# Kernel optimization log

Hardware: AMD Instinct MI355X
Metric: run time of the kernel (lower is better)

The kernel has to match this reference:

```python
import jax, jax.numpy as jnp
import numpy as np

L_OBS = 512                      # number_of_obs
FOV = 6.283185307179586          # full 360-degree scan
EPS_PAR = 1e-4                   # parallel-ray threshold (matches torch |rxs|<0.0001)
MAP_SIZE = 256.0
B = 8
N = 8192


def setup_inputs() -> dict:
    key = jax.random.key(0)
    k1, k2, k3 = jax.random.split(key, 3)
    # map line segments: (x3, y3, x4, y4) in [0, 256]^2
    line_seg = jax.random.uniform(k1, (N, 4), dtype=jnp.float32) * MAP_SIZE
    # poses: xy in the map interior, theta in [0, 2pi)
    xy = MAP_SIZE * 0.25 + jax.random.uniform(k2, (B, 2), dtype=jnp.float32) * (MAP_SIZE * 0.5)
    theta = jax.random.uniform(k3, (B, 1), dtype=jnp.float32) * (2.0 * np.pi)
    pose = jnp.concatenate([xy, theta], axis=-1)
    return {"line_seg": line_seg, "pose": pose}


def _sense(line_seg, pose):
    # rays(): beam angles for each pose -> [B, L]
    beam = jnp.arange(L_OBS, dtype=jnp.float32) * (FOV / L_OBS)        # [L]
    ang = beam[None, :] + pose[:, 2:3]                                  # [B, L]
    rx = jnp.cos(ang)[:, :, None]                                       # [B, L, 1]
    ry = jnp.sin(ang)[:, :, None]
    x1 = pose[:, 0][:, None, None]                                      # [B, 1, 1]
    y1 = pose[:, 1][:, None, None]

    x3 = line_seg[:, 0][None, None, :]                                  # [1, 1, N]
    y3 = line_seg[:, 1][None, None, :]
    x4 = line_seg[:, 2][None, None, :]
    y4 = line_seg[:, 3][None, None, :]
    sx = x4 - x3
    sy = y4 - y3
    x1_x3 = x1 - x3                                                     # [B, 1, N]
    y1_y3 = y1 - y3

    # ray/segment intersection parameters, broadcast to [B, L, N]
    num_a = sx * y1_y3 - sy * x1_x3
    num_b = rx * y1_y3 - ry * x1_x3
    rxs = sy * rx - sx * ry
    parallel = jnp.abs(rxs) < EPS_PAR
    safe_rxs = jnp.where(parallel, jnp.float32(1.0), rxs)
    u_a = jnp.where(parallel, jnp.float32(0.0), num_a / safe_rxs)       # [B, L, N]
    u_b = jnp.where(parallel, jnp.float32(0.0), num_b / safe_rxs)

    valid = (~parallel) & (u_b >= 0.0) & (u_b <= 1.0) & (u_a >= 0.0)
    # nearest valid hit along each ray (torch: +1e7 penalty then nanargmin)
    u_masked = jnp.where(valid, u_a, jnp.float32(jnp.inf))
    idx = jnp.argmin(u_masked, axis=-1)                                 # [B, L]
    u_sel = jnp.take_along_axis(u_a, idx[:, :, None], axis=-1)          # [B, L, 1]

    ix = x1[:, :, 0] + rx[:, :, 0] * u_sel[:, :, 0]                     # [B, L]
    iy = y1[:, :, 0] + ry[:, :, 0] * u_sel[:, :, 0]
    return jnp.stack([ix, iy], axis=-1)                                 # [B, L, 2]


def _to_sensor_frame(pose, obs_global):
    c0 = pose[:, None, 0:2]                                             # [B, 1, 2]
    cos = jnp.cos(pose[:, 2])
    sin = jnp.sin(pose[:, 2])
    # R = [[cos, -sin], [sin, cos]] per batch, obs_local = (obs - c0) @ R
    R = jnp.stack([jnp.stack([cos, -sin], -1), jnp.stack([sin, cos], -1)], -2)  # [B, 2, 2]
    return jnp.einsum('blj,bjk->blk', obs_global - c0, R)


def reference(line_seg, pose):
    obs_global = _sense(line_seg, pose)
    obs_local = _to_sensor_frame(pose, obs_global)
    return obs_global, obs_local
```

## Files before the change

### kernel.cpp

```cpp
#include <hip/hip_runtime.h>
#include <math.h>

#define L_OBS   512
#define NSEG    8192
#define NB      8
#define EPS_PAR 1e-4f
#define ANG_STEP 0.012271846644580566f
#define INV_STEP 81.48733086305042f
#define PI_F     3.14159265358979f
#define TWOPI_F  6.28318530717959f
#define INV_2PI  0.15915494309189535f
#define MARG     2e-3f

#define SC2   32
#define CSEG2 (NSEG / SC2)
#define PART2_FLOATS (SC2 * NB * L_OBS)

__global__ __launch_bounds__(512) void raycast10_kernel(
    const float4* __restrict__ seg, const float* __restrict__ pose,
    float* __restrict__ part) {
    __shared__ float4 s4[CSEG2];
    __shared__ float  s_red[8][128];
    __shared__ int    s_n;

    const int gid = blockIdx.x;
    const int sc = gid & (SC2 - 1);
    const int bg = (gid >> 5) & 3;
    const int b  = gid >> 7;

    const float x1 = pose[b * 3 + 0];
    const float y1 = pose[b * 3 + 1];
    const float th = pose[b * 3 + 2];

    const int t = threadIdx.x;
    if (t == 0) s_n = 0;
    __syncthreads();

    if (t < CSEG2) {
        float4 v = seg[sc * CSEG2 + t];
        float aA = atan2f(v.y - y1, v.x - x1);
        float aB = atan2f(v.w - y1, v.z - x1);
        float d  = aB - aA;
        if (d > PI_F) d -= TWOPI_F; else if (d < -PI_F) d += TWOPI_F;
        float lo  = (d >= 0.0f) ? aA : aB;
        float wdt = fabsf(d);

        bool keep;
        if (wdt > PI_F - 0.02f) {
            keep = true;
        } else {
            float a = lo - th;
            a -= floorf(a * INV_2PI) * TWOPI_F;
            int ilo = (int)floorf((a - MARG) * INV_STEP);
            int ihi = (int)floorf((a + wdt + MARG) * INV_STEP) + 1;
            if (ilo < 0) { ilo += 512; ihi += 512; }
            const int B0 = bg * 128, B1 = bg * 128 + 127;
            keep = (ilo <= B1 && ihi >= B0) || (ihi >= B0 + 512);
        }
        if (keep) {
            int pos = atomicAdd(&s_n, 1);
            s4[pos] = make_float4(v.z - v.x, v.w - v.y, x1 - v.x, y1 - v.y);
        }
    }

    const int lane = t & 63;
    const int w    = t >> 6;
    const int beam0 = bg * 128 + lane;
    const float a0 = (float)beam0 * ANG_STEP + th;
    const float a1 = (float)(beam0 + 64) * ANG_STEP + th;
    const float rx0 = cosf(a0), ry0 = sinf(a0);
    const float rx1 = cosf(a1), ry1 = sinf(a1);
    const float INF = __builtin_inff();
    __syncthreads();

    const int n = s_n;
    float u0 = INF, u1 = INF;
    #pragma unroll 4
    for (int i = w; i < n; i += 8) {
        float4 s = s4[i];
        float na = s.x * s.w - s.y * s.z;

        float rxs0 = s.y * rx0 - s.x * ry0;
        float nb0  = rx0 * s.w - ry0 * s.z;
        float r0   = __builtin_amdgcn_rcpf(rxs0);
        float ua0  = na  * r0;
        float ub0  = nb0 * r0;
        bool ok0 = (fabsf(rxs0) >= EPS_PAR) & (ub0 >= 0.0f) & (ub0 <= 1.0f) & (ua0 >= 0.0f);
        u0 = fminf(u0, ok0 ? ua0 : INF);

        float rxs1 = s.y * rx1 - s.x * ry1;
        float nb1  = rx1 * s.w - ry1 * s.z;
        float r1   = __builtin_amdgcn_rcpf(rxs1);
        float ua1  = na  * r1;
        float ub1  = nb1 * r1;
        bool ok1 = (fabsf(rxs1) >= EPS_PAR) & (ub1 >= 0.0f) & (ub1 <= 1.0f) & (ua1 >= 0.0f);
        u1 = fminf(u1, ok1 ? ua1 : INF);
    }

    s_red[w][lane]      = u0;
    s_red[w][lane + 64] = u1;
    __syncthreads();
    if (t < 128) {
        float m0 = fminf(fminf(s_red[0][t], s_red[1][t]),
                         fminf(s_red[2][t], s_red[3][t]));
        float m1 = fminf(fminf(s_red[4][t], s_red[5][t]),
                         fminf(s_red[6][t], s_red[7][t]));
        part[sc * (NB * L_OBS) + b * L_OBS + bg * 128 + t] = fminf(m0, m1);
    }
}

__global__ __launch_bounds__(256) void finalize7_kernel(
    const float4* __restrict__ seg, const float* __restrict__ pose,
    const float* __restrict__ part, float* __restrict__ out) {
    __shared__ float s_red[4][64];

    const int t    = threadIdx.x;
    const int lane = t & 63;
    const int q    = t >> 6;
    const int gbeam = blockIdx.x * 64 + lane;

    float u = INFINITY;
    #pragma unroll
    for (int j = 0; j < 8; ++j)
        u = fminf(u, part[(q * 8 + j) * (NB * L_OBS) + gbeam]);

    s_red[q][lane] = u;
    __syncthreads();
    if (t < 64) {
        const int gb   = blockIdx.x * 64 + t;
        const int b    = gb >> 9;
        const int beam = gb & (L_OBS - 1);
        const float x1 = pose[b * 3 + 0];
        const float y1 = pose[b * 3 + 1];
        const float th = pose[b * 3 + 2];
        const float ang = (float)beam * ANG_STEP + th;
        const float rx = cosf(ang), ry = sinf(ang);

        float m = fminf(fminf(s_red[0][t], s_red[1][t]),
                        fminf(s_red[2][t], s_red[3][t]));

        if (isinf(m)) {
            float4 s0 = seg[0];
            float sx = s0.z - s0.x, sy = s0.w - s0.y;
            float xd = x1 - s0.x,   yd = y1 - s0.y;
            float rxs   = sy * rx - sx * ry;
            float num_a = sx * yd - sy * xd;
            m = (fabsf(rxs) < EPS_PAR) ? 0.0f : (num_a / rxs);
        }

        float ix = x1 + rx * m;
        float iy = y1 + ry * m;
        float dx = ix - x1, dy = iy - y1;
        float c = cosf(th), s = sinf(th);
        out[gb * 2 + 0] = ix;
        out[gb * 2 + 1] = iy;
        const int off = NB * L_OBS * 2;
        out[off + gb * 2 + 0] =  dx * c + dy * s;
        out[off + gb * 2 + 1] = -dx * s + dy * c;
    }
}

extern "C" void kernel_launch(void* const* d_in, const int* in_sizes, int n_in,
                              void* d_out, int out_size, void* d_ws, size_t ws_size,
                              hipStream_t stream) {
    const float4* seg  = (const float4*)d_in[0];
    const float*  pose = (const float*)d_in[1];
    float* out = (float*)d_out;
    float* part = (float*)d_ws;

    raycast10_kernel<<<1024, 512, 0, stream>>>(seg, pose, part);
    finalize7_kernel<<<64, 256, 0, stream>>>(seg, pose, part, out);
}
```

Measured before the change: 19.01 us.

## Fuse raycast and finalize into one kernel with fine 16-beam culling

Replaces the two-kernel split-and-reduce scheme with a single kernel where each block handles 16 beams of one pose and streams all segments in 16 chunks, culling each chunk by angular range before intersecting. This removes the workspace round trip and the second launch, and the narrower beam window culls more segments. In exchange, every block recomputes atan2 culling over all segments, adding many more transcendental evaluations and barriers per block, with fewer blocks overall.

```diff
diff --git a/kernel.cpp b/kernel.cpp
--- a/kernel.cpp
+++ b/kernel.cpp
@@ -12,146 +12,110 @@
 #define INV_2PI  0.15915494309189535f
 #define MARG     2e-3f
 
-#define SC2   32
-#define CSEG2 (NSEG / SC2)
-#define PART2_FLOATS (SC2 * NB * L_OBS)
+#define NCHK   16
+#define CHKSZ  (NSEG / NCHK)
 
-__global__ __launch_bounds__(512) void raycast10_kernel(
+__global__ __launch_bounds__(1024) void raycast11_kernel(
     const float4* __restrict__ seg, const float* __restrict__ pose,
-    float* __restrict__ part) {
-    __shared__ float4 s4[CSEG2];
-    __shared__ float  s_red[8][128];
-    __shared__ int    s_n;
+    float* __restrict__ out) {
+    __shared__ float4 s4[CHKSZ];
+    __shared__ float  red[16][16];
+    __shared__ int    s_cnt[NCHK];
 
-    const int gid = blockIdx.x;
-    const int sc = gid & (SC2 - 1);
-    const int bg = (gid >> 5) & 3;
-    const int b  = gid >> 7;
+    const int g   = blockIdx.x;
+    const int b   = g >> 5;
+    const int grp = g & 31;
+    const int t   = threadIdx.x;
+    const int bm    = t & 15;
+    const int slice = t >> 4;
+    const int w     = t >> 6;
 
     const float x1 = pose[b * 3 + 0];
     const float y1 = pose[b * 3 + 1];
     const float th = pose[b * 3 + 2];
+    const int   B0 = grp << 4;
+    const int   B1 = B0 + 15;
 
-    const int t = threadIdx.x;
-    if (t == 0) s_n = 0;
+    const int beam = B0 + bm;
+    const float ang = (float)beam * ANG_STEP + th;
+    const float rx = cosf(ang), ry = sinf(ang);
+    const float INF = __builtin_inff();
+
+    if (t < NCHK) s_cnt[t] = 0;
     __syncthreads();
 
-    if (t < CSEG2) {
-        float4 v = seg[sc * CSEG2 + t];
-        float aA = atan2f(v.y - y1, v.x - x1);
-        float aB = atan2f(v.w - y1, v.z - x1);
-        float d  = aB - aA;
-        if (d > PI_F) d -= TWOPI_F; else if (d < -PI_F) d += TWOPI_F;
-        float lo  = (d >= 0.0f) ? aA : aB;
-        float wdt = fabsf(d);
+    float umin = INF;
+    for (int c = 0; c < NCHK; ++c) {
+        if (t < CHKSZ) {
+            float4 v = seg[(c << 9) + t];
+            float aA = atan2f(v.y - y1, v.x - x1);
+            float aB = atan2f(v.w - y1, v.z - x1);
+            float d  = aB - aA;
+            if (d > PI_F) d -= TWOPI_F; else if (d < -PI_F) d += TWOPI_F;
+            float lo  = (d >= 0.0f) ? aA : aB;
+            float wdt = fabsf(d);
 
-        bool keep;
-        if (wdt > PI_F - 0.02f) {
-            keep = true;
-        } else {
-            float a = lo - th;
-            a -= floorf(a * INV_2PI) * TWOPI_F;
-            int ilo = (int)floorf((a - MARG) * INV_STEP);
-            int ihi = (int)floorf((a + wdt + MARG) * INV_STEP) + 1;
-            if (ilo < 0) { ilo += 512; ihi += 512; }
-            const int B0 = bg * 128, B1 = bg * 128 + 127;
-            keep = (ilo <= B1 && ihi >= B0) || (ihi >= B0 + 512);
+            bool keep;
+            if (wdt > PI_F - 0.02f) {
+                keep = true;
+            } else {
+                float a = lo - th;
+                a -= floorf(a * INV_2PI) * TWOPI_F;
+                int ilo = (int)floorf((a - MARG) * INV_STEP);
+                int ihi = (int)floorf((a + wdt + MARG) * INV_STEP) + 1;
+                if (ilo < 0) { ilo += 512; ihi += 512; }
+                keep = (ilo <= B1 && ihi >= B0) || (ihi >= B0 + 512);
+            }
+            if (keep) {
+                int pos = atomicAdd(&s_cnt[c], 1);
+                s4[pos] = make_float4(v.z - v.x, v.w - v.y, x1 - v.x, y1 - v.y);
+            }
         }
-        if (keep) {
-            int pos = atomicAdd(&s_n, 1);
-            s4[pos] = make_float4(v.z - v.x, v.w - v.y, x1 - v.x, y1 - v.y);
+        __syncthreads();
+
+        const int n = s_cnt[c];
+        for (int i = slice; i < n; i += 64) {
+            float4 s = s4[i];
+            float rxs = s.y * rx - s.x * ry;
+            float na  = s.x * s.w - s.y * s.z;
+            float nb  = rx * s.w - ry * s.z;
+            float r   = __builtin_amdgcn_rcpf(rxs);
+            float ua  = na * r;
+            float ub  = nb * r;
+            bool ok = (fabsf(rxs) >= EPS_PAR) & (ub >= 0.0f) & (ub <= 1.0f) & (ua >= 0.0f);
+            umin = fminf(umin, ok ? ua : INF);
         }
+        __syncthreads();
     }
 
-    const int lane = t & 63;
-    const int w    = t >> 6;
-    const int beam0 = bg * 128 + lane;
-    const float a0 = (float)beam0 * ANG_STEP + th;
-    const float a1 = (float)(beam0 + 64) * ANG_STEP + th;
-    const float rx0 = cosf(a0), ry0 = sinf(a0);
-    const float rx1 = cosf(a1), ry1 = sinf(a1);
-    const float INF = __builtin_inff();
+    umin = fminf(umin, __shfl_xor(umin, 16));
+    umin = fminf(umin, __shfl_xor(umin, 32));
+    if ((t & 63) < 16) red[w][bm] = umin;
     __syncthreads();
 
-    const int n = s_n;
-    float u0 = INF, u1 = INF;
-    #pragma unroll 4
-    for (int i = w; i < n; i += 8) {
-        float4 s = s4[i];
-        float na = s.x * s.w - s.y * s.z;
+    if (t < 16) {
+        float m = red[0][t];
+        #pragma unroll
+        for (int j = 1; j < 16; ++j) m = fminf(m, red[j][t]);
 
-        float rxs0 = s.y * rx0 - s.x * ry0;
-        float nb0  = rx0 * s.w - ry0 * s.z;
-        float r0   = __builtin_amdgcn_rcpf(rxs0);
-        float ua0  = na  * r0;
-        float ub0  = nb0 * r0;
-        bool ok0 = (fabsf(rxs0) >= EPS_PAR) & (ub0 >= 0.0f) & (ub0 <= 1.0f) & (ua0 >= 0.0f);
-        u0 = fminf(u0, ok0 ? ua0 : INF);
-
-        float rxs1 = s.y * rx1 - s.x * ry1;
-        float nb1  = rx1 * s.w - ry1 * s.z;
-        float r1   = __builtin_amdgcn_rcpf(rxs1);
-        float ua1  = na  * r1;
-        float ub1  = nb1 * r1;
-        bool ok1 = (fabsf(rxs1) >= EPS_PAR) & (ub1 >= 0.0f) & (ub1 <= 1.0f) & (ua1 >= 0.0f);
-        u1 = fminf(u1, ok1 ? ua1 : INF);
-    }
-
-    s_red[w][lane]      = u0;
-    s_red[w][lane + 64] = u1;
-    __syncthreads();
-    if (t < 128) {
-        float m0 = fminf(fminf(s_red[0][t], s_red[1][t]),
-                         fminf(s_red[2][t], s_red[3][t]));
-        float m1 = fminf(fminf(s_red[4][t], s_red[5][t]),
-                         fminf(s_red[6][t], s_red[7][t]));
-        part[sc * (NB * L_OBS) + b * L_OBS + bg * 128 + t] = fminf(m0, m1);
-    }
-}
-
-__global__ __launch_bounds__(256) void finalize7_kernel(
-    const float4* __restrict__ seg, const float* __restrict__ pose,
-    const float* __restrict__ part, float* __restrict__ out) {
-    __shared__ float s_red[4][64];
-
-    const int t    = threadIdx.x;
-    const int lane = t & 63;
-    const int q    = t >> 6;
-    const int gbeam = blockIdx.x * 64 + lane;
-
-    float u = INFINITY;
-    #pragma unroll
-    for (int j = 0; j < 8; ++j)
-        u = fminf(u, part[(q * 8 + j) * (NB * L_OBS) + gbeam]);
-
-    s_red[q][lane] = u;
-    __syncthreads();
-    if (t < 64) {
-        const int gb   = blockIdx.x * 64 + t;
-        const int b    = gb >> 9;
-        const int beam = gb & (L_OBS - 1);
-        const float x1 = pose[b * 3 + 0];
-        const float y1 = pose[b * 3 + 1];
-        const float th = pose[b * 3 + 2];
-        const float ang = (float)beam * ANG_STEP + th;
-        const float rx = cosf(ang), ry = sinf(ang);
-
-        float m = fminf(fminf(s_red[0][t], s_red[1][t]),
-                        fminf(s_red[2][t], s_red[3][t]));
+        const int gbeam = B0 + t;
+        const float angf = (float)gbeam * ANG_STEP + th;
+        const float rxf = cosf(angf), ryf = sinf(angf);
 
         if (isinf(m)) {
             float4 s0 = seg[0];
             float sx = s0.z - s0.x, sy = s0.w - s0.y;
             float xd = x1 - s0.x,   yd = y1 - s0.y;
-            float rxs   = sy * rx - sx * ry;
+            float rxs   = sy * rxf - sx * ryf;
             float num_a = sx * yd - sy * xd;
             m = (fabsf(rxs) < EPS_PAR) ? 0.0f : (num_a / rxs);
         }
 
-        float ix = x1 + rx * m;
-        float iy = y1 + ry * m;
+        float ix = x1 + rxf * m;
+        float iy = y1 + ryf * m;
         float dx = ix - x1, dy = iy - y1;
         float c = cosf(th), s = sinf(th);
+        const int gb = b * L_OBS + gbeam;
         out[gb * 2 + 0] = ix;
         out[gb * 2 + 1] = iy;
         const int off = NB * L_OBS * 2;
@@ -166,8 +130,6 @@
     const float4* seg  = (const float4*)d_in[0];
     const float*  pose = (const float*)d_in[1];
     float* out = (float*)d_out;
-    float* part = (float*)d_ws;
 
-    raycast10_kernel<<<1024, 512, 0, stream>>>(seg, pose, part);
-    finalize7_kernel<<<64, 256, 0, stream>>>(seg, pose, part, out);
+    raycast11_kernel<<<NB * 32, 1024, 0, stream>>>(seg, pose, out);
 }
```

Result: slower. 30.26 us (+59.2%).
